# Optimization experiments

Hardware: AMD Instinct MI355X
Metric: run time of the kernel (lower is better)

The kernel has to match this reference:

```python
import jax, jax.numpy as jnp
import numpy as np

N_NODES = 50000
N_EDGES = 800000
D_FEAT = 128
D_HID = 128
N_CLASSES = 16


def setup_inputs() -> dict:
    key = jax.random.key(0)
    ks = jax.random.split(key, 5)
    x = jax.random.normal(ks[0], (N_NODES, D_FEAT), dtype=jnp.float32)
    edge_index = jax.random.randint(ks[1], (2, N_EDGES), 0, N_NODES, dtype=jnp.int32)
    # Glorot-ish scaled weights to keep activations in a sane range
    W1 = jax.random.normal(ks[2], (D_FEAT, D_HID), dtype=jnp.float32) * 0.05
    b1 = jnp.zeros((D_HID,), dtype=jnp.float32)
    W2 = jax.random.normal(ks[3], (D_HID, N_CLASSES), dtype=jnp.float32) * 0.05
    b2 = jnp.zeros((N_CLASSES,), dtype=jnp.float32)
    return {"x": x, "edge_index": edge_index, "W1": W1, "b1": b1, "W2": W2, "b2": b2}


def _gcn_conv(h, src, dst, norm, W, b, num_nodes):
    # linear transform first (F_in >= F_out ordering as in PyG GCNConv)
    h = h @ W                              # [N, F_out]
    msg = h[src] * norm[:, None]           # gather + edge-wise scale  [E+N, F_out]
    out = jax.ops.segment_sum(msg, dst, num_segments=num_nodes)  # scatter-add
    return out + b


def reference(x, edge_index, W1, b1, W2, b2):
    n = x.shape[0]
    loop = jnp.arange(n, dtype=edge_index.dtype)
    src = jnp.concatenate([edge_index[0], loop])  # add self-loops
    dst = jnp.concatenate([edge_index[1], loop])
    # symmetric normalization: deg^{-1/2}[src] * deg^{-1/2}[dst]
    deg = jax.ops.segment_sum(jnp.ones_like(dst, dtype=x.dtype), dst, num_segments=n)
    dis = jax.lax.rsqrt(jnp.maximum(deg, 1.0))  # deg >= 1 thanks to self-loops
    norm = dis[src] * dis[dst]
    h = jax.nn.relu(_gcn_conv(x, src, dst, norm, W1, b1, n))
    # dropout is identity in eval mode
    out = _gcn_conv(h, src, dst, norm, W2, b2, n)
    return jax.nn.sigmoid(out)
```

## Files before the change

### kernel.cpp

```cpp
#include <hip/hip_runtime.h>
#include <math.h>

#define NN 50000
#define NE 800000
#define DF 128
#define NC 16
#define WLD 136
#define NBIN 196
#define EPB 2048
#define HB ((NE + EPB - 1) / EPB)
#define HL (NBIN * HB)
#define PB ((HL + 255) / 256)
#define GB ((NN + 63) / 64)

typedef __bf16 bf16x8 __attribute__((ext_vector_type(8)));
typedef __bf16 bf16x4 __attribute__((ext_vector_type(4)));
typedef float  f32x4  __attribute__((ext_vector_type(4)));

__global__ void k_prep(const float* __restrict__ W1, const float* __restrict__ W2,
                       __bf16* __restrict__ W1T, __bf16* __restrict__ W2T) {
    int i = blockIdx.x * blockDim.x + threadIdx.x;
    if (i < DF * DF) {
        int n = i >> 7, k = i & 127;
        W1T[i] = (__bf16)W1[k * DF + n];
    }
    int j = i - DF * DF;
    if (j >= 0 && j < NC * DF) {
        int n = j >> 7, k = j & 127;
        W2T[j] = (__bf16)W2[k * NC + n];
    }
}

__global__ __launch_bounds__(256) void k_gemm1_hist(const float* __restrict__ X,
                                                    const __bf16* __restrict__ W1T,
                                                    __bf16* __restrict__ H1,
                                                    const int* __restrict__ dst,
                                                    int* __restrict__ h) {
    __shared__ __bf16 wlds[DF * WLD];
    __shared__ int hc[NBIN];
    if (blockIdx.x >= GB) {
        const int bb = blockIdx.x - GB;
        const int t = threadIdx.x;
        if (t < NBIN) hc[t] = 0;
        __syncthreads();
        const int base = bb * EPB;
#pragma unroll
        for (int i = 0; i < EPB / 256; ++i) {
            int e = base + i * 256 + t;
            if (e < NE) atomicAdd(&hc[dst[e] >> 8], 1);
        }
        __syncthreads();
        if (t < NBIN) h[t * HB + bb] = hc[t];
        return;
    }
    const int wid = threadIdx.x >> 6, lane = threadIdx.x & 63;
    const int m0 = blockIdx.x * 64 + wid * 16;
    const int m = m0 + (lane & 15);
    const int mc = (m < NN) ? m : NN - 1;
    const int l15 = lane & 15;
    const int kb = (lane >> 4) * 8;

    float4 xf[8];
#pragma unroll
    for (int q = 0; q < 4; ++q) {
        xf[2 * q]     = *(const float4*)&X[(size_t)mc * DF + q * 32 + kb];
        xf[2 * q + 1] = *(const float4*)&X[(size_t)mc * DF + q * 32 + kb + 4];
    }
    for (int i = threadIdx.x; i < DF * 16; i += 256) {
        int row = i >> 4, c8 = i & 15;
        *(bf16x8*)&wlds[row * WLD + c8 * 8] = ((const bf16x8*)W1T)[i];
    }
    __syncthreads();

    f32x4 acc[8];
#pragma unroll
    for (int nf = 0; nf < 8; ++nf) acc[nf] = (f32x4){0.f, 0.f, 0.f, 0.f};
#pragma unroll
    for (int ks = 0; ks < 4; ++ks) {
        float4 x0 = xf[2 * ks], x1 = xf[2 * ks + 1];
        bf16x8 xa;
        xa[0] = (__bf16)x0.x; xa[1] = (__bf16)x0.y; xa[2] = (__bf16)x0.z; xa[3] = (__bf16)x0.w;
        xa[4] = (__bf16)x1.x; xa[5] = (__bf16)x1.y; xa[6] = (__bf16)x1.z; xa[7] = (__bf16)x1.w;
#pragma unroll
        for (int nf = 0; nf < 8; ++nf) {
            bf16x8 wa = *(const bf16x8*)&wlds[(nf * 16 + l15) * WLD + ks * 32 + kb];
            acc[nf] = __builtin_amdgcn_mfma_f32_16x16x32_bf16(wa, xa, acc[nf], 0, 0, 0);
        }
    }
    if (m < NN) {
#pragma unroll
        for (int nf = 0; nf < 8; ++nf) {
            bf16x4 o;
            o[0] = (__bf16)acc[nf][0]; o[1] = (__bf16)acc[nf][1];
            o[2] = (__bf16)acc[nf][2]; o[3] = (__bf16)acc[nf][3];
            *(bf16x4*)&H1[(size_t)m * DF + nf * 16 + (lane >> 4) * 4] = o;
        }
    }
}

__global__ __launch_bounds__(256) void k_hpart(const int* __restrict__ h,
                                               int* __restrict__ part) {
    __shared__ int ws[4];
    const int b = blockIdx.x, t = threadIdx.x;
    const int idx = b * 256 + t;
    int s = (idx < HL) ? h[idx] : 0;
    for (int o = 32; o > 0; o >>= 1) s += __shfl_down(s, o);
    if ((t & 63) == 0) ws[t >> 6] = s;
    __syncthreads();
    if (t == 0) part[b] = ws[0] + ws[1] + ws[2] + ws[3];
}

__global__ __launch_bounds__(512) void k_hscan_part(const int* __restrict__ part,
                                                    int* __restrict__ partoff,
                                                    int* __restrict__ hscan) {
    __shared__ int s[512];
    const int t = threadIdx.x;
    int v = (t < PB) ? part[t] : 0;
    s[t] = v;
    __syncthreads();
    for (int o = 1; o < 512; o <<= 1) {
        int x = (t >= o) ? s[t - o] : 0;
        __syncthreads();
        s[t] += x;
        __syncthreads();
    }
    if (t < PB) partoff[t] = s[t] - v;
    if (t == 511) hscan[HL] = s[511];
}

__global__ __launch_bounds__(256) void k_hoff(const int* __restrict__ h,
                                              const int* __restrict__ partoff,
                                              int* __restrict__ hscan) {
    __shared__ int s[256];
    const int b = blockIdx.x, t = threadIdx.x;
    const int idx = b * 256 + t;
    int v = (idx < HL) ? h[idx] : 0;
    s[t] = v;
    __syncthreads();
    for (int o = 1; o < 256; o <<= 1) {
        int x = (t >= o) ? s[t - o] : 0;
        __syncthreads();
        s[t] += x;
        __syncthreads();
    }
    if (idx < HL) hscan[idx] = partoff[b] + s[t] - v;
}

__global__ __launch_bounds__(256) void k_scatterA(const int* __restrict__ src,
                                                  const int* __restrict__ dst,
                                                  const int* __restrict__ hscan,
                                                  int2* __restrict__ ebuf) {
    __shared__ int cur[NBIN];
    const int bb = blockIdx.x, t = threadIdx.x;
    if (t < NBIN) cur[t] = hscan[t * HB + bb];
    __syncthreads();
    const int base = bb * EPB;
#pragma unroll
    for (int i = 0; i < EPB / 256; ++i) {
        int e = base + i * 256 + t;
        if (e < NE) {
            int s = src[e], d = dst[e];
            int pos = atomicAdd(&cur[d >> 8], 1);
            ebuf[pos] = make_int2(s, d);
        }
    }
}

__global__ __launch_bounds__(256) void k_rankB(const int2* __restrict__ ebuf,
                                               const int* __restrict__ hscan,
                                               int* __restrict__ off,
                                               float* __restrict__ dis,
                                               int* __restrict__ rec) {
    __shared__ int cnt[256], s[256], cur[256];
    const int bin = blockIdx.x, t = threadIdx.x;
    const int base = hscan[bin * HB];
    const int end  = hscan[(bin + 1) * HB];
    cnt[t] = 0;
    __syncthreads();
    for (int e = base + t; e < end; e += 256)
        atomicAdd(&cnt[ebuf[e].y & 255], 1);
    __syncthreads();
    int c = cnt[t];
    s[t] = c;
    __syncthreads();
    for (int o = 1; o < 256; o <<= 1) {
        int x = (t >= o) ? s[t - o] : 0;
        __syncthreads();
        s[t] += x;
        __syncthreads();
    }
    int lo = s[t] - c;
    int d = (bin << 8) + t;
    if (d < NN) {
        off[d] = base + lo;
        dis[d] = rsqrtf((float)(c + 1));
    }
    if (bin == NBIN - 1 && t == 0) off[NN] = NE;
    cur[t] = base + lo;
    __syncthreads();
    for (int e = base + t; e < end; e += 256) {
        int2 ed = ebuf[e];
        int p = atomicAdd(&cur[ed.y & 255], 1);
        rec[p] = ed.x;
    }
}

__global__ __launch_bounds__(256) void k_agg1g2(const __bf16* __restrict__ H1,
                                                const float* __restrict__ dis,
                                                const float* __restrict__ b1,
                                                const __bf16* __restrict__ W2T,
                                                const int* __restrict__ off,
                                                const int* __restrict__ rec,
                                                float* __restrict__ H2) {
    const int wid = threadIdx.x >> 6, lane = threadIdx.x & 63;
    const int n = blockIdx.x * 4 + wid;
    if (n >= NN) return;
    const int g = lane >> 4, l16 = lane & 15;
    const int fo = l16 * 8;
    const float dn = dis[n];

    float a[8];
    if (g == 0) {
        float d2 = dn * dn;
        float4 b0 = *(const float4*)&b1[fo];
        float4 b4 = *(const float4*)&b1[fo + 4];
        bf16x8 hs = *(const bf16x8*)&H1[(size_t)n * DF + fo];
        a[0] = b0.x + (float)hs[0] * d2;
        a[1] = b0.y + (float)hs[1] * d2;
        a[2] = b0.z + (float)hs[2] * d2;
        a[3] = b0.w + (float)hs[3] * d2;
        a[4] = b4.x + (float)hs[4] * d2;
        a[5] = b4.y + (float)hs[5] * d2;
        a[6] = b4.z + (float)hs[6] * d2;
        a[7] = b4.w + (float)hs[7] * d2;
    } else {
#pragma unroll
        for (int i = 0; i < 8; ++i) a[i] = 0.f;
    }

    const int e0 = off[n], e1 = off[n + 1];
    int e = e0 + g;
    for (; e + 4 < e1; e += 8) {
        int r0 = rec[e];
        int r1 = rec[e + 4];
        float w0 = dis[r0] * dn;
        float w1 = dis[r1] * dn;
        bf16x8 h0 = *(const bf16x8*)&H1[(size_t)r0 * DF + fo];
        bf16x8 h1 = *(const bf16x8*)&H1[(size_t)r1 * DF + fo];
#pragma unroll
        for (int i = 0; i < 8; ++i) a[i] += (float)h0[i] * w0;
#pragma unroll
        for (int i = 0; i < 8; ++i) a[i] += (float)h1[i] * w1;
    }
    for (; e < e1; e += 4) {
        int r = rec[e];
        float w = dis[r] * dn;
        bf16x8 h = *(const bf16x8*)&H1[(size_t)r * DF + fo];
#pragma unroll
        for (int i = 0; i < 8; ++i) a[i] += (float)h[i] * w;
    }
#pragma unroll
    for (int i = 0; i < 8; ++i) {
        a[i] += __shfl_xor(a[i], 16);
        a[i] += __shfl_xor(a[i], 32);
        a[i] = fmaxf(a[i], 0.f);
    }

    float p[4];
#pragma unroll
    for (int j = 0; j < 4; ++j) {
        bf16x8 wr = *(const bf16x8*)&W2T[(size_t)(g * 4 + j) * DF + fo];
        float s = 0.f;
#pragma unroll
        for (int i = 0; i < 8; ++i) s += a[i] * (float)wr[i];
        p[j] = s;
    }
#pragma unroll
    for (int o = 1; o <= 8; o <<= 1) {
#pragma unroll
        for (int j = 0; j < 4; ++j) p[j] += __shfl_xor(p[j], o);
    }
    if (l16 == 0) {
        f32x4 o4 = {p[0], p[1], p[2], p[3]};
        *(f32x4*)&H2[(size_t)n * NC + g * 4] = o4;
    }
}

__global__ __launch_bounds__(256) void k_agg2(const float* __restrict__ H2,
                                              const float* __restrict__ dis,
                                              const float* __restrict__ b2,
                                              const int* __restrict__ off,
                                              const int* __restrict__ rec,
                                              float* __restrict__ OUT) {
    const int wid = threadIdx.x >> 6, lane = threadIdx.x & 63;
    const int n = blockIdx.x * 4 + wid;
    if (n >= NN) return;
    const float dn = dis[n];

    const int g = lane >> 3, l8 = lane & 7;
    float ax = 0.f, ay = 0.f;
    const int e0 = off[n], e1 = off[n + 1];
    for (int e = e0 + g; e < e1; e += 8) {
        int r = rec[e];
        float w = dis[r] * dn;
        float2 h = *(const float2*)&H2[(size_t)r * NC + l8 * 2];
        ax += h.x * w;
        ay += h.y * w;
    }
    ax += __shfl_xor(ax, 8);  ay += __shfl_xor(ay, 8);
    ax += __shfl_xor(ax, 16); ay += __shfl_xor(ay, 16);
    ax += __shfl_xor(ax, 32); ay += __shfl_xor(ay, 32);
    if (g == 0) {
        float d2 = dn * dn;
        float2 hs = *(const float2*)&H2[(size_t)n * NC + l8 * 2];
        float2 bb = *(const float2*)&b2[l8 * 2];
        float vx = bb.x + hs.x * d2 + ax;
        float vy = bb.y + hs.y * d2 + ay;
        float2 o = { 1.0f / (1.0f + expf(-vx)), 1.0f / (1.0f + expf(-vy)) };
        *(float2*)&OUT[(size_t)n * NC + l8 * 2] = o;
    }
}

extern "C" void kernel_launch(void* const* d_in, const int* in_sizes, int n_in,
                              void* d_out, int out_size, void* d_ws, size_t ws_size,
                              hipStream_t stream) {
    const float* X  = (const float*)d_in[0];
    const int*   EI = (const int*)d_in[1];
    const float* W1 = (const float*)d_in[2];
    const float* b1 = (const float*)d_in[3];
    const float* W2 = (const float*)d_in[4];
    const float* b2 = (const float*)d_in[5];
    float* OUT = (float*)d_out;

    const int* src = EI;
    const int* dst = EI + NE;

    char* ws = (char*)d_ws;
    int*    h       = (int*)(ws);
    int*    hscan   = (int*)(ws + 327680);
    int*    hpart   = (int*)(ws + 655360);
    int*    hpartoff= (int*)(ws + 659456);
    int*    off     = (int*)(ws + 663552);
    float*  dis     = (float*)(ws + 868352);
    __bf16* W1T     = (__bf16*)(ws + 1073152);
    __bf16* W2T     = (__bf16*)(ws + 1105920);
    int2*   ebuf    = (int2*)(ws + 1110016);
    int*    rec     = (int*)(ws + 7510016);
    __bf16* H1      = (__bf16*)(ws + 10710016);
    float*  H2      = (float*)(ws + 23510016);

    const int B = 256;

    k_prep<<<(DF * DF + NC * DF + B - 1) / B, B, 0, stream>>>(W1, W2, W1T, W2T);
    k_gemm1_hist<<<GB + HB, B, 0, stream>>>(X, W1T, H1, dst, h);
    k_hpart<<<PB, B, 0, stream>>>(h, hpart);
    k_hscan_part<<<1, 512, 0, stream>>>(hpart, hpartoff, hscan);
    k_hoff<<<PB, B, 0, stream>>>(h, hpartoff, hscan);
    k_scatterA<<<HB, B, 0, stream>>>(src, dst, hscan, ebuf);
    k_rankB<<<NBIN, B, 0, stream>>>(ebuf, hscan, off, dis, rec);

    k_agg1g2<<<(NN + 3) / 4, B, 0, stream>>>(H1, dis, b1, W2T, off, rec, H2);
    k_agg2<<<(NN + 3) / 4, B, 0, stream>>>(H2, dis, b2, off, rec, OUT);
}
```

Baseline: 110.3 us.

## Pack edge buffers to 16-bit sources, hoist norm scaling, unroll gathers

The intermediate edge buffer is packed from int2 to a single int: the source index sits in the low 16 bits and the low byte of the destination in bits 16-23. The CSR neighbor list is stored as unsigned short, which is valid because the node count stays below 65536. This halves sort and neighbor-index traffic across the scatter, rank and both aggregation kernels. The per-edge multiply by the destination's normalization factor is moved after the loop, and the gather loops are unrolled further (4 rows in layer 1, 2 in layer 2) to keep more loads in flight. The 16-bit packing ties the code to graphs with fewer than 65536 nodes.

```diff
diff --git a/kernel.cpp b/kernel.cpp
--- a/kernel.cpp
+++ b/kernel.cpp
@@ -149,7 +149,7 @@
 __global__ __launch_bounds__(256) void k_scatterA(const int* __restrict__ src,
                                                   const int* __restrict__ dst,
                                                   const int* __restrict__ hscan,
-                                                  int2* __restrict__ ebuf) {
+                                                  int* __restrict__ ebuf) {
     __shared__ int cur[NBIN];
     const int bb = blockIdx.x, t = threadIdx.x;
     if (t < NBIN) cur[t] = hscan[t * HB + bb];
@@ -161,16 +161,16 @@
         if (e < NE) {
             int s = src[e], d = dst[e];
             int pos = atomicAdd(&cur[d >> 8], 1);
-            ebuf[pos] = make_int2(s, d);
+            ebuf[pos] = s | ((d & 255) << 16);
         }
     }
 }
 
-__global__ __launch_bounds__(256) void k_rankB(const int2* __restrict__ ebuf,
+__global__ __launch_bounds__(256) void k_rankB(const int* __restrict__ ebuf,
                                                const int* __restrict__ hscan,
                                                int* __restrict__ off,
                                                float* __restrict__ dis,
-                                               int* __restrict__ rec) {
+                                               unsigned short* __restrict__ rec) {
     __shared__ int cnt[256], s[256], cur[256];
     const int bin = blockIdx.x, t = threadIdx.x;
     const int base = hscan[bin * HB];
@@ -178,7 +178,7 @@
     cnt[t] = 0;
     __syncthreads();
     for (int e = base + t; e < end; e += 256)
-        atomicAdd(&cnt[ebuf[e].y & 255], 1);
+        atomicAdd(&cnt[(ebuf[e] >> 16) & 255], 1);
     __syncthreads();
     int c = cnt[t];
     s[t] = c;
@@ -199,9 +199,9 @@
     cur[t] = base + lo;
     __syncthreads();
     for (int e = base + t; e < end; e += 256) {
-        int2 ed = ebuf[e];
-        int p = atomicAdd(&cur[ed.y & 255], 1);
-        rec[p] = ed.x;
+        int ed = ebuf[e];
+        int p = atomicAdd(&cur[(ed >> 16) & 255], 1);
+        rec[p] = (unsigned short)(ed & 0xFFFF);
     }
 }
 
@@ -210,7 +210,7 @@
                                                 const float* __restrict__ b1,
                                                 const __bf16* __restrict__ W2T,
                                                 const int* __restrict__ off,
-                                                const int* __restrict__ rec,
+                                                const unsigned short* __restrict__ rec,
                                                 float* __restrict__ H2) {
     const int wid = threadIdx.x >> 6, lane = threadIdx.x & 63;
     const int n = blockIdx.x * 4 + wid;
@@ -220,50 +220,55 @@
     const float dn = dis[n];
 
     float a[8];
-    if (g == 0) {
-        float d2 = dn * dn;
+#pragma unroll
+    for (int i = 0; i < 8; ++i) a[i] = 0.f;
+
+    const int e0 = off[n], e1 = off[n + 1];
+    int e = e0 + g;
+    for (; e + 12 < e1; e += 16) {
+        int r0 = rec[e];
+        int r1 = rec[e + 4];
+        int r2 = rec[e + 8];
+        int r3 = rec[e + 12];
+        float w0 = dis[r0], w1 = dis[r1], w2 = dis[r2], w3 = dis[r3];
+        bf16x8 h0 = *(const bf16x8*)&H1[(size_t)r0 * DF + fo];
+        bf16x8 h1 = *(const bf16x8*)&H1[(size_t)r1 * DF + fo];
+        bf16x8 h2 = *(const bf16x8*)&H1[(size_t)r2 * DF + fo];
+        bf16x8 h3 = *(const bf16x8*)&H1[(size_t)r3 * DF + fo];
+#pragma unroll
+        for (int i = 0; i < 8; ++i) a[i] += (float)h0[i] * w0;
+#pragma unroll
+        for (int i = 0; i < 8; ++i) a[i] += (float)h1[i] * w1;
+#pragma unroll
+        for (int i = 0; i < 8; ++i) a[i] += (float)h2[i] * w2;
+#pragma unroll
+        for (int i = 0; i < 8; ++i) a[i] += (float)h3[i] * w3;
+    }
+    for (; e < e1; e += 4) {
+        int r = rec[e];
+        float w = dis[r];
+        bf16x8 h = *(const bf16x8*)&H1[(size_t)r * DF + fo];
+#pragma unroll
+        for (int i = 0; i < 8; ++i) a[i] += (float)h[i] * w;
+    }
+#pragma unroll
+    for (int i = 0; i < 8; ++i) {
+        a[i] += __shfl_xor(a[i], 16);
+        a[i] += __shfl_xor(a[i], 32);
+    }
+    {
+        const float d2 = dn * dn;
         float4 b0 = *(const float4*)&b1[fo];
         float4 b4 = *(const float4*)&b1[fo + 4];
         bf16x8 hs = *(const bf16x8*)&H1[(size_t)n * DF + fo];
-        a[0] = b0.x + (float)hs[0] * d2;
-        a[1] = b0.y + (float)hs[1] * d2;
-        a[2] = b0.z + (float)hs[2] * d2;
-        a[3] = b0.w + (float)hs[3] * d2;
-        a[4] = b4.x + (float)hs[4] * d2;
-        a[5] = b4.y + (float)hs[5] * d2;
-        a[6] = b4.z + (float)hs[6] * d2;
-        a[7] = b4.w + (float)hs[7] * d2;
-    } else {
-#pragma unroll
-        for (int i = 0; i < 8; ++i) a[i] = 0.f;
-    }
-
-    const int e0 = off[n], e1 = off[n + 1];
-    int e = e0 + g;
-    for (; e + 4 < e1; e += 8) {
-        int r0 = rec[e];
-        int r1 = rec[e + 4];
-        float w0 = dis[r0] * dn;
-        float w1 = dis[r1] * dn;
-        bf16x8 h0 = *(const bf16x8*)&H1[(size_t)r0 * DF + fo];
-        bf16x8 h1 = *(const bf16x8*)&H1[(size_t)r1 * DF + fo];
-#pragma unroll
-        for (int i = 0; i < 8; ++i) a[i] += (float)h0[i] * w0;
-#pragma unroll
-        for (int i = 0; i < 8; ++i) a[i] += (float)h1[i] * w1;
-    }
-    for (; e < e1; e += 4) {
-        int r = rec[e];
-        float w = dis[r] * dn;
-        bf16x8 h = *(const bf16x8*)&H1[(size_t)r * DF + fo];
-#pragma unroll
-        for (int i = 0; i < 8; ++i) a[i] += (float)h[i] * w;
-    }
-#pragma unroll
-    for (int i = 0; i < 8; ++i) {
-        a[i] += __shfl_xor(a[i], 16);
-        a[i] += __shfl_xor(a[i], 32);
-        a[i] = fmaxf(a[i], 0.f);
+        a[0] = fmaxf(a[0] * dn + (float)hs[0] * d2 + b0.x, 0.f);
+        a[1] = fmaxf(a[1] * dn + (float)hs[1] * d2 + b0.y, 0.f);
+        a[2] = fmaxf(a[2] * dn + (float)hs[2] * d2 + b0.z, 0.f);
+        a[3] = fmaxf(a[3] * dn + (float)hs[3] * d2 + b0.w, 0.f);
+        a[4] = fmaxf(a[4] * dn + (float)hs[4] * d2 + b4.x, 0.f);
+        a[5] = fmaxf(a[5] * dn + (float)hs[5] * d2 + b4.y, 0.f);
+        a[6] = fmaxf(a[6] * dn + (float)hs[6] * d2 + b4.z, 0.f);
+        a[7] = fmaxf(a[7] * dn + (float)hs[7] * d2 + b4.w, 0.f);
     }
 
     float p[4];
@@ -290,7 +295,7 @@
                                               const float* __restrict__ dis,
                                               const float* __restrict__ b2,
                                               const int* __restrict__ off,
-                                              const int* __restrict__ rec,
+                                              const unsigned short* __restrict__ rec,
                                               float* __restrict__ OUT) {
     const int wid = threadIdx.x >> 6, lane = threadIdx.x & 63;
     const int n = blockIdx.x * 4 + wid;
@@ -300,9 +305,21 @@
     const int g = lane >> 3, l8 = lane & 7;
     float ax = 0.f, ay = 0.f;
     const int e0 = off[n], e1 = off[n + 1];
-    for (int e = e0 + g; e < e1; e += 8) {
+    int e = e0 + g;
+    for (; e + 8 < e1; e += 16) {
+        int r0 = rec[e];
+        int r1 = rec[e + 8];
+        float w0 = dis[r0], w1 = dis[r1];
+        float2 h0 = *(const float2*)&H2[(size_t)r0 * NC + l8 * 2];
+        float2 h1 = *(const float2*)&H2[(size_t)r1 * NC + l8 * 2];
+        ax += h0.x * w0;
+        ay += h0.y * w0;
+        ax += h1.x * w1;
+        ay += h1.y * w1;
+    }
+    for (; e < e1; e += 8) {
         int r = rec[e];
-        float w = dis[r] * dn;
+        float w = dis[r];
         float2 h = *(const float2*)&H2[(size_t)r * NC + l8 * 2];
         ax += h.x * w;
         ay += h.y * w;
@@ -314,8 +331,8 @@
         float d2 = dn * dn;
         float2 hs = *(const float2*)&H2[(size_t)n * NC + l8 * 2];
         float2 bb = *(const float2*)&b2[l8 * 2];
-        float vx = bb.x + hs.x * d2 + ax;
-        float vy = bb.y + hs.y * d2 + ay;
+        float vx = ax * dn + hs.x * d2 + bb.x;
+        float vy = ay * dn + hs.y * d2 + bb.y;
         float2 o = { 1.0f / (1.0f + expf(-vx)), 1.0f / (1.0f + expf(-vy)) };
         *(float2*)&OUT[(size_t)n * NC + l8 * 2] = o;
     }
@@ -344,10 +361,10 @@
     float*  dis     = (float*)(ws + 868352);
     __bf16* W1T     = (__bf16*)(ws + 1073152);
     __bf16* W2T     = (__bf16*)(ws + 1105920);
-    int2*   ebuf    = (int2*)(ws + 1110016);
-    int*    rec     = (int*)(ws + 7510016);
-    __bf16* H1      = (__bf16*)(ws + 10710016);
-    float*  H2      = (float*)(ws + 23510016);
+    int*    ebuf    = (int*)(ws + 1110016);
+    unsigned short* rec = (unsigned short*)(ws + 4310016);
+    __bf16* H1      = (__bf16*)(ws + 5910016);
+    float*  H2      = (float*)(ws + 18710016);
 
     const int B = 256;
 
```

After: 104.5 us. 1.06x faster.
